# Performance work log

Hardware: AMD Instinct MI355X
Metric: run time of the kernel (lower is better)

Reference implementation:

```python
import jax, jax.numpy as jnp
import numpy as np

N_NODES = 100000
N_EDGES = 1600000
IN_C, HID_C, OUT_C = 128, 128, 64


def gcn_conv(x, src, dst, W, b, num_nodes):
    # PyG GCNConv: add self-loops, symmetric normalization, linear transform,
    # aggregate source features into targets.
    h = x @ W  # [N, C_out]
    loop = jnp.arange(num_nodes, dtype=src.dtype)
    s = jnp.concatenate([src, loop])
    d = jnp.concatenate([dst, loop])
    deg = jax.ops.segment_sum(jnp.ones_like(d, dtype=h.dtype), d, num_segments=num_nodes)
    inv_sqrt = jnp.where(deg > 0, jax.lax.rsqrt(deg), 0.0)
    norm = inv_sqrt[s] * inv_sqrt[d]  # [E+N]
    msgs = h[s] * norm[:, None]  # gather + scale
    out = jax.ops.segment_sum(msgs, d, num_segments=num_nodes)  # scatter-add
    return out + b


def setup_inputs() -> dict:
    key = jax.random.key(0)
    k1, k2, k3, k4 = jax.random.split(key, 4)
    x = jax.random.normal(k1, (N_NODES, IN_C), dtype=jnp.float32)
    edge_index = jax.random.randint(k2, (2, N_EDGES), 0, N_NODES, dtype=jnp.int64)
    W1 = jax.random.normal(k3, (IN_C, HID_C), dtype=jnp.float32) * (1.0 / np.sqrt(IN_C))
    b1 = jnp.zeros((HID_C,), dtype=jnp.float32)
    W2 = jax.random.normal(k4, (HID_C, OUT_C), dtype=jnp.float32) * (1.0 / np.sqrt(HID_C))
    b2 = jnp.zeros((OUT_C,), dtype=jnp.float32)
    return {"x": x, "edge_index": edge_index, "W1": W1, "b1": b1, "W2": W2, "b2": b2}


def reference(x, edge_index, W1, b1, W2, b2):
    num_nodes = x.shape[0]
    src, dst = edge_index[0], edge_index[1]  # PyG flow: source -> target
    h = gcn_conv(x, src, dst, W1, b1, num_nodes)
    h = jax.nn.relu(h)  # dropout is identity in eval mode
    out = gcn_conv(h, src, dst, W2, b2, num_nodes)
    return out
```

## Files before the change

kernel.cpp:

```cpp
#include <hip/hip_runtime.h>

#define IN_C 128
#define HID_C 128
#define OUT_C 64

#define BSPAN 256
#define BCAP  5120
#define NBMAX 512
#define ACHUNK 4096

typedef unsigned int uint32;
typedef unsigned short ushort16;
typedef _Float16 f16;
typedef f16   f16x8 __attribute__((ext_vector_type(8)));
typedef float f32x4 __attribute__((ext_vector_type(4)));


__device__ __forceinline__ ushort16 f2bf(float f) {
    union { float f; uint32 u; } v; v.f = f;
    uint32 r = v.u + 0x7FFFu + ((v.u >> 16) & 1u);
    return (ushort16)(r >> 16);
}

__device__ __forceinline__ void unpack2(uint32 u, float& f0, float& f1) {
    union { uint32 x; float f; } a, b;
    a.x = u << 16;
    b.x = u & 0xFFFF0000u;
    f0 = a.f; f1 = b.f;
}


__launch_bounds__(256)
__global__ void bin_edges_kernel(const int* __restrict__ src, const int* __restrict__ dst,
                                 int* __restrict__ bucketCur, uint32* __restrict__ binned,
                                 int E, int nbuck) {
    __shared__ int hist[NBMAX];
    __shared__ int base[NBMAX];
    __shared__ int rank[NBMAX];
    const int tid = threadIdx.x;
    const int e0  = blockIdx.x * ACHUNK;

    for (int i = tid; i < NBMAX; i += 256) { hist[i] = 0; rank[i] = 0; }
    __syncthreads();

    int d[16], s[16];
#pragma unroll
    for (int j = 0; j < 16; j++) {
        int e = e0 + j * 256 + tid;
        if (e < E) {
            d[j] = dst[e];
            s[j] = src[e];
            atomicAdd(&hist[d[j] >> 8], 1);
        } else d[j] = -1;
    }
    __syncthreads();

    for (int b = tid; b < nbuck; b += 256) {
        int h = hist[b];
        base[b] = h ? atomicAdd(&bucketCur[b], h) : 0;
    }
    __syncthreads();

#pragma unroll
    for (int j = 0; j < 16; j++) {
        if (d[j] >= 0) {
            int b = d[j] >> 8;
            int r = atomicAdd(&rank[b], 1);
            int pos = base[b] + r;
            if (pos < BCAP)
                binned[(size_t)b * BCAP + pos] =
                    ((uint32)(d[j] & 255) << 17) | (uint32)s[j];
        }
    }
}


__launch_bounds__(256)
__global__ void bucket_csr_kernel(const uint32* __restrict__ binned,
                                  const int* __restrict__ bucketCur,
                                  int* __restrict__ csr_src, int* __restrict__ rowbeg,
                                  int* __restrict__ rowend, float* __restrict__ inv, int N) {
    __shared__ int cnt[BSPAN];
    __shared__ int scn[BSPAN];
    __shared__ int cur[BSPAN];
    const int b   = blockIdx.x;
    const int tid = threadIdx.x;
    const int n0  = b * BSPAN;
    const int ne  = min(bucketCur[b], BCAP);
    const uint32* bp = binned + (size_t)b * BCAP;

    cnt[tid] = 0;
    __syncthreads();
    for (int i = tid; i < ne; i += 256)
        atomicAdd(&cnt[bp[i] >> 17], 1);
    __syncthreads();

    int v = cnt[tid];
    scn[tid] = v;
    __syncthreads();
    for (int off = 1; off < 256; off <<= 1) {
        int u = (tid >= off) ? scn[tid - off] : 0;
        __syncthreads();
        scn[tid] += u;
        __syncthreads();
    }
    int excl = scn[tid] - v;
    cur[tid] = excl;

    int n = n0 + tid;
    if (n < N) {
        int gb = b * BCAP + excl;
        rowbeg[n] = gb;
        rowend[n] = gb + v;
        inv[n] = rsqrtf((float)(v + 1));
    }
    __syncthreads();

    for (int i = tid; i < ne; i += 256) {
        uint32 e = bp[i];
        int r = atomicAdd(&cur[e >> 17], 1);
        csr_src[(size_t)b * BCAP + r] = (int)(e & 0x1FFFFu);
    }
}


template <int C>
__global__ void wprep_kernel(const float* __restrict__ W, f16* __restrict__ Wf) {
    constexpr int NCT = C / 16;
    int t = blockIdx.x * 256 + threadIdx.x;
    if (t >= 4 * NCT * 64) return;
    int lane = t & 63;
    int ctkc = t >> 6;
    int ct = ctkc % NCT, kc = ctkc / NCT;
    int kbase = kc * 32 + (lane >> 4) * 8;
    int col   = ct * 16 + (lane & 15);
    f16 v[8];
#pragma unroll
    for (int j = 0; j < 8; j++) v[j] = (f16)W[(size_t)(kbase + j) * C + col];
    *(uint4*)(Wf + (size_t)t * 8) = *(const uint4*)v;
}


template <int C, bool AF16>
__launch_bounds__(256)
__global__ void mfma_gemm(const void* __restrict__ Xv, const f16* __restrict__ Wf,
                          const float* __restrict__ inv, ushort16* __restrict__ outb, int N) {
    constexpr int NCT = C / 16;
    __shared__ __align__(16) f16 As[4 * 4 * 64 * 8];
    __shared__ __align__(16) f16 Bs[4 * NCT * 64 * 8];

    const int tid  = threadIdx.x;
    const int lane = tid & 63;
    const int w    = tid >> 6;
    const int row0 = blockIdx.x * 64;

    {
        constexpr int TOT = 4 * NCT * 64 * 8;
        const uint4* src = (const uint4*)Wf;
        uint4* dst = (uint4*)Bs;
#pragma unroll
        for (int i = 0; i < TOT / 8 / 256; i++)
            dst[tid + i * 256] = src[tid + i * 256];
    }

    {
        int r   = tid >> 2;
        int seg = tid & 3;
        int row = row0 + r;
        int ws_ = r >> 4;
        int r15 = r & 15;
        if (!AF16) {
            const float* X = (const float*)Xv;
#pragma unroll
            for (int i = 0; i < 8; i++) {
                int k = seg * 32 + i * 4;
                float4 v = make_float4(0.f, 0.f, 0.f, 0.f);
                if (row < N) v = *(const float4*)(X + (size_t)row * 128 + k);
                int q = (k >> 3) & 3, j0 = k & 7;
                f16 h[4] = {(f16)v.x, (f16)v.y, (f16)v.z, (f16)v.w};
                int slot = ((seg * 4 + ws_) * 64 + (q * 16 + r15)) * 8 + j0;
                *(uint2*)(As + slot) = *(const uint2*)h;
            }
        } else {
            const f16* X = (const f16*)Xv;
#pragma unroll
            for (int i = 0; i < 4; i++) {
                int k = seg * 32 + i * 8;
                uint4 v = make_uint4(0, 0, 0, 0);
                if (row < N) v = *(const uint4*)(X + (size_t)row * 128 + k);
                int q = (k >> 3) & 3;
                int slot = ((seg * 4 + ws_) * 64 + (q * 16 + r15)) * 8;
                *(uint4*)(As + slot) = v;
            }
        }
    }
    __syncthreads();

    f32x4 acc[NCT];
#pragma unroll
    for (int c = 0; c < NCT; c++) acc[c] = (f32x4){0.f, 0.f, 0.f, 0.f};

#pragma unroll
    for (int kc = 0; kc < 4; kc++) {
        f16x8 a = *(const f16x8*)&As[((kc * 4 + w) * 64 + lane) * 8];
#pragma unroll
        for (int ct = 0; ct < NCT; ct++) {
            f16x8 b = *(const f16x8*)&Bs[((kc * NCT + ct) * 64 + lane) * 8];
            acc[ct] = __builtin_amdgcn_mfma_f32_16x16x32_f16(a, b, acc[ct], 0, 0, 0);
        }
    }

    __syncthreads();
    ushort16* Ds = (ushort16*)As;
    const int q = lane >> 4;
    float iv[4];
#pragma unroll
    for (int reg = 0; reg < 4; reg++) {
        int row = row0 + w * 16 + q * 4 + reg;
        iv[reg] = (row < N) ? inv[row] : 0.f;
    }
#pragma unroll
    for (int ct = 0; ct < NCT; ct++) {
#pragma unroll
        for (int reg = 0; reg < 4; reg++) {
            int r = w * 16 + q * 4 + reg;
            Ds[r * C + ct * 16 + (lane & 15)] = f2bf(acc[ct][reg] * iv[reg]);
        }
    }
    __syncthreads();
    {
        int r  = tid >> 2;
        int row = row0 + r;
        if (row < N) {
            constexpr int SPT = C / 4;
            int c0 = (tid & 3) * SPT;
            const uint4* s = (const uint4*)&Ds[r * C + c0];
            uint4* d = (uint4*)(outb + (size_t)row * C + c0);
#pragma unroll
            for (int i = 0; i < SPT / 8; i++) d[i] = s[i];
        }
    }
}


template <int C, bool RELU, bool F16OUT>
__launch_bounds__(256)
__global__ void gather_agg_bf16(const int* __restrict__ rowbeg, const int* __restrict__ rowend,
                                const int* __restrict__ csr_src,
                                const ushort16* __restrict__ hsb, const float* __restrict__ inv,
                                const float* __restrict__ b, void* __restrict__ outv, int N) {
    constexpr int TPN = C / 8;
    constexpr int NPB = 256 / TPN;
    int n    = blockIdx.x * NPB + threadIdx.x / TPN;
    int lane = threadIdx.x % TPN;
    if (n >= N) return;
    int c8 = lane * 8;

    float acc[8];
    {
        uint4 raw = *(const uint4*)(hsb + (size_t)n * C + c8);
        unpack2(raw.x, acc[0], acc[1]);
        unpack2(raw.y, acc[2], acc[3]);
        unpack2(raw.z, acc[4], acc[5]);
        unpack2(raw.w, acc[6], acc[7]);
    }

    int beg = rowbeg[n];
    int end = rowend[n];
    int i = beg;
    for (; i + 2 <= end; i += 2) {
        int s0 = csr_src[i];
        int s1 = csr_src[i + 1];
        uint4 r0 = *(const uint4*)(hsb + (size_t)s0 * C + c8);
        uint4 r1 = *(const uint4*)(hsb + (size_t)s1 * C + c8);
        float f0, f1;
        unpack2(r0.x, f0, f1); acc[0] += f0; acc[1] += f1;
        unpack2(r0.y, f0, f1); acc[2] += f0; acc[3] += f1;
        unpack2(r0.z, f0, f1); acc[4] += f0; acc[5] += f1;
        unpack2(r0.w, f0, f1); acc[6] += f0; acc[7] += f1;
        unpack2(r1.x, f0, f1); acc[0] += f0; acc[1] += f1;
        unpack2(r1.y, f0, f1); acc[2] += f0; acc[3] += f1;
        unpack2(r1.z, f0, f1); acc[4] += f0; acc[5] += f1;
        unpack2(r1.w, f0, f1); acc[6] += f0; acc[7] += f1;
    }
    if (i < end) {
        int s0 = csr_src[i];
        uint4 r0 = *(const uint4*)(hsb + (size_t)s0 * C + c8);
        float f0, f1;
        unpack2(r0.x, f0, f1); acc[0] += f0; acc[1] += f1;
        unpack2(r0.y, f0, f1); acc[2] += f0; acc[3] += f1;
        unpack2(r0.z, f0, f1); acc[4] += f0; acc[5] += f1;
        unpack2(r0.w, f0, f1); acc[6] += f0; acc[7] += f1;
    }

    float iv = inv[n];
    float4 b0 = *(const float4*)(b + c8);
    float4 b1 = *(const float4*)(b + c8 + 4);
    float r[8];
    r[0] = fmaf(iv, acc[0], b0.x); r[1] = fmaf(iv, acc[1], b0.y);
    r[2] = fmaf(iv, acc[2], b0.z); r[3] = fmaf(iv, acc[3], b0.w);
    r[4] = fmaf(iv, acc[4], b1.x); r[5] = fmaf(iv, acc[5], b1.y);
    r[6] = fmaf(iv, acc[6], b1.z); r[7] = fmaf(iv, acc[7], b1.w);
    if (RELU) {
#pragma unroll
        for (int j = 0; j < 8; j++) r[j] = fmaxf(r[j], 0.f);
    }
    if (F16OUT) {
        f16 o[8];
#pragma unroll
        for (int j = 0; j < 8; j++) o[j] = (f16)r[j];
        *(uint4*)((f16*)outv + (size_t)n * C + c8) = *(const uint4*)o;
    } else {
        float* po = (float*)outv + (size_t)n * C + c8;
        *(float4*)(po)     = make_float4(r[0], r[1], r[2], r[3]);
        *(float4*)(po + 4) = make_float4(r[4], r[5], r[6], r[7]);
    }
}

extern "C" void kernel_launch(void* const* d_in, const int* in_sizes, int n_in,
                              void* d_out, int out_size, void* d_ws, size_t ws_size,
                              hipStream_t stream) {
    const float* x  = (const float*)d_in[0];
    const int*   ei = (const int*)d_in[1];
    const float* W1 = (const float*)d_in[2];
    const float* b1 = (const float*)d_in[3];
    const float* W2 = (const float*)d_in[4];
    const float* b2 = (const float*)d_in[5];
    float* out = (float*)d_out;

    const int N = in_sizes[0] / IN_C;
    const int E = in_sizes[1] / 2;
    const int* src = ei;
    const int* dst = ei + E;
    const int nbuck = (N + BSPAN - 1) / BSPAN;

    char* ws = (char*)d_ws;
    auto align_up = [](size_t v) { return (v + 1023) & ~(size_t)1023; };
    size_t off = 0;
    int*      bucketCur = (int*)(ws + off);      off += align_up((size_t)nbuck * sizeof(int));
    float*    inv       = (float*)(ws + off);    off += align_up((size_t)N * sizeof(float));
    int*      rowbeg    = (int*)(ws + off);      off += align_up((size_t)N * sizeof(int));
    int*      rowend    = (int*)(ws + off);      off += align_up((size_t)N * sizeof(int));
    uint32*   binned    = (uint32*)(ws + off);   off += align_up((size_t)nbuck * BCAP * sizeof(uint32));
    int*      csrs      = (int*)(ws + off);      off += align_up((size_t)nbuck * BCAP * sizeof(int));
    f16*      Wf1       = (f16*)(ws + off);      off += align_up((size_t)4 * (HID_C/16) * 64 * 8 * sizeof(f16));
    f16*      Wf2       = (f16*)(ws + off);      off += align_up((size_t)4 * (OUT_C/16) * 64 * 8 * sizeof(f16));
    ushort16* hs1b      = (ushort16*)(ws + off); off += align_up((size_t)N * HID_C * sizeof(ushort16));
    f16*      h1post    = (f16*)(ws + off);      off += align_up((size_t)N * HID_C * sizeof(f16));
    ushort16* hs2b      = (ushort16*)(ws + off); off += align_up((size_t)N * OUT_C * sizeof(ushort16));

    hipMemsetAsync(bucketCur, 0, (size_t)nbuck * sizeof(int), stream);
    wprep_kernel<HID_C><<<(4 * (HID_C/16) * 64 + 255) / 256, 256, 0, stream>>>(W1, Wf1);
    wprep_kernel<OUT_C><<<(4 * (OUT_C/16) * 64 + 255) / 256, 256, 0, stream>>>(W2, Wf2);
    bin_edges_kernel<<<(E + ACHUNK - 1) / ACHUNK, 256, 0, stream>>>(
        src, dst, bucketCur, binned, E, nbuck);
    bucket_csr_kernel<<<nbuck, 256, 0, stream>>>(
        binned, bucketCur, csrs, rowbeg, rowend, inv, N);

    mfma_gemm<HID_C, false><<<(N + 63) / 64, 256, 0, stream>>>(x, Wf1, inv, hs1b, N);
    {
        constexpr int NPB = 256 / (HID_C / 8);
        gather_agg_bf16<HID_C, true, true><<<(N + NPB - 1) / NPB, 256, 0, stream>>>(
            rowbeg, rowend, csrs, hs1b, inv, b1, h1post, N);
    }

    mfma_gemm<OUT_C, true><<<(N + 63) / 64, 256, 0, stream>>>(h1post, Wf2, inv, hs2b, N);
    {
        constexpr int NPB = 256 / (OUT_C / 8);
        gather_agg_bf16<OUT_C, false, false><<<(N + NPB - 1) / NPB, 256, 0, stream>>>(
            rowbeg, rowend, csrs, hs2b, inv, b2, out, N);
    }
}
```

Measured before the change: 271.6 us.

## Reuse atomic ranks in binning and CSR, merge weight prep, unroll gather by four

The binning kernel now keeps the rank returned by the histogram atomic, which removes the second shared-memory atomic pass. The bucket CSR kernel buffers each thread's edges and ranks in registers, so it skips re-reading the binned array and the second atomic pass. The two weight-prep launches are merged into one kernel, and the gather loop is unrolled to four rows per step to keep more loads in flight. The per-thread buffers (20 entries) add register pressure, and edge order within a row becomes nondeterministic, which can slightly change float summation order.

```diff
diff --git a/kernel.cpp b/kernel.cpp
--- a/kernel.cpp
+++ b/kernel.cpp
@@ -36,21 +36,20 @@
                                  int E, int nbuck) {
     __shared__ int hist[NBMAX];
     __shared__ int base[NBMAX];
-    __shared__ int rank[NBMAX];
     const int tid = threadIdx.x;
     const int e0  = blockIdx.x * ACHUNK;
 
-    for (int i = tid; i < NBMAX; i += 256) { hist[i] = 0; rank[i] = 0; }
-    __syncthreads();
-
-    int d[16], s[16];
+    for (int i = tid; i < NBMAX; i += 256) hist[i] = 0;
+    __syncthreads();
+
+    int d[16], s[16], rk[16];
 #pragma unroll
     for (int j = 0; j < 16; j++) {
         int e = e0 + j * 256 + tid;
         if (e < E) {
             d[j] = dst[e];
             s[j] = src[e];
-            atomicAdd(&hist[d[j] >> 8], 1);
+            rk[j] = atomicAdd(&hist[d[j] >> 8], 1);
         } else d[j] = -1;
     }
     __syncthreads();
@@ -65,8 +64,7 @@
     for (int j = 0; j < 16; j++) {
         if (d[j] >= 0) {
             int b = d[j] >> 8;
-            int r = atomicAdd(&rank[b], 1);
-            int pos = base[b] + r;
+            int pos = base[b] + rk[j];
             if (pos < BCAP)
                 binned[(size_t)b * BCAP + pos] =
                     ((uint32)(d[j] & 255) << 17) | (uint32)s[j];
@@ -80,9 +78,10 @@
                                   const int* __restrict__ bucketCur,
                                   int* __restrict__ csr_src, int* __restrict__ rowbeg,
                                   int* __restrict__ rowend, float* __restrict__ inv, int N) {
+    constexpr int MAXIT = BCAP / 256;
     __shared__ int cnt[BSPAN];
     __shared__ int scn[BSPAN];
-    __shared__ int cur[BSPAN];
+    __shared__ int excl[BSPAN];
     const int b   = blockIdx.x;
     const int tid = threadIdx.x;
     const int n0  = b * BSPAN;
@@ -91,8 +90,16 @@
 
     cnt[tid] = 0;
     __syncthreads();
-    for (int i = tid; i < ne; i += 256)
-        atomicAdd(&cnt[bp[i] >> 17], 1);
+
+    uint32 ebuf[MAXIT];
+    int    rbuf[MAXIT];
+    int nmine = 0;
+    for (int i = tid; i < ne; i += 256) {
+        uint32 e = bp[i];
+        ebuf[nmine] = e;
+        rbuf[nmine] = atomicAdd(&cnt[e >> 17], 1);
+        nmine++;
+    }
     __syncthreads();
 
     int v = cnt[tid];
@@ -104,31 +111,28 @@
         scn[tid] += u;
         __syncthreads();
     }
-    int excl = scn[tid] - v;
-    cur[tid] = excl;
+    int ex = scn[tid] - v;
+    excl[tid] = ex;
 
     int n = n0 + tid;
     if (n < N) {
-        int gb = b * BCAP + excl;
+        int gb = b * BCAP + ex;
         rowbeg[n] = gb;
         rowend[n] = gb + v;
         inv[n] = rsqrtf((float)(v + 1));
     }
     __syncthreads();
 
-    for (int i = tid; i < ne; i += 256) {
-        uint32 e = bp[i];
-        int r = atomicAdd(&cur[e >> 17], 1);
-        csr_src[(size_t)b * BCAP + r] = (int)(e & 0x1FFFFu);
+    for (int j = 0; j < nmine; j++) {
+        uint32 e = ebuf[j];
+        csr_src[(size_t)b * BCAP + excl[e >> 17] + rbuf[j]] = (int)(e & 0x1FFFFu);
     }
 }
 
 
 template <int C>
-__global__ void wprep_kernel(const float* __restrict__ W, f16* __restrict__ Wf) {
+__device__ __forceinline__ void wprep_one(const float* __restrict__ W, f16* __restrict__ Wf, int t) {
     constexpr int NCT = C / 16;
-    int t = blockIdx.x * 256 + threadIdx.x;
-    if (t >= 4 * NCT * 64) return;
     int lane = t & 63;
     int ctkc = t >> 6;
     int ct = ctkc % NCT, kc = ctkc / NCT;
@@ -138,6 +142,15 @@
 #pragma unroll
     for (int j = 0; j < 8; j++) v[j] = (f16)W[(size_t)(kbase + j) * C + col];
     *(uint4*)(Wf + (size_t)t * 8) = *(const uint4*)v;
+}
+
+__global__ void wprep_both(const float* __restrict__ W1, f16* __restrict__ Wf1,
+                           const float* __restrict__ W2, f16* __restrict__ Wf2) {
+    constexpr int T1 = 4 * (HID_C / 16) * 64;
+    constexpr int T2 = 4 * (OUT_C / 16) * 64;
+    int t = blockIdx.x * 256 + threadIdx.x;
+    if (t < T1)            wprep_one<HID_C>(W1, Wf1, t);
+    else if (t < T1 + T2)  wprep_one<OUT_C>(W2, Wf2, t - T1);
 }
 
 
@@ -242,6 +255,14 @@
     }
 }
 
+
+__device__ __forceinline__ void acc_row(uint4 r, float* acc) {
+    float f0, f1;
+    unpack2(r.x, f0, f1); acc[0] += f0; acc[1] += f1;
+    unpack2(r.y, f0, f1); acc[2] += f0; acc[3] += f1;
+    unpack2(r.z, f0, f1); acc[4] += f0; acc[5] += f1;
+    unpack2(r.w, f0, f1); acc[6] += f0; acc[7] += f1;
+}
 
 template <int C, bool RELU, bool F16OUT>
 __launch_bounds__(256)
@@ -268,29 +289,21 @@
     int beg = rowbeg[n];
     int end = rowend[n];
     int i = beg;
-    for (; i + 2 <= end; i += 2) {
+    for (; i + 4 <= end; i += 4) {
         int s0 = csr_src[i];
         int s1 = csr_src[i + 1];
+        int s2 = csr_src[i + 2];
+        int s3 = csr_src[i + 3];
         uint4 r0 = *(const uint4*)(hsb + (size_t)s0 * C + c8);
         uint4 r1 = *(const uint4*)(hsb + (size_t)s1 * C + c8);
-        float f0, f1;
-        unpack2(r0.x, f0, f1); acc[0] += f0; acc[1] += f1;
-        unpack2(r0.y, f0, f1); acc[2] += f0; acc[3] += f1;
-        unpack2(r0.z, f0, f1); acc[4] += f0; acc[5] += f1;
-        unpack2(r0.w, f0, f1); acc[6] += f0; acc[7] += f1;
-        unpack2(r1.x, f0, f1); acc[0] += f0; acc[1] += f1;
-        unpack2(r1.y, f0, f1); acc[2] += f0; acc[3] += f1;
-        unpack2(r1.z, f0, f1); acc[4] += f0; acc[5] += f1;
-        unpack2(r1.w, f0, f1); acc[6] += f0; acc[7] += f1;
-    }
-    if (i < end) {
+        uint4 r2 = *(const uint4*)(hsb + (size_t)s2 * C + c8);
+        uint4 r3 = *(const uint4*)(hsb + (size_t)s3 * C + c8);
+        acc_row(r0, acc); acc_row(r1, acc); acc_row(r2, acc); acc_row(r3, acc);
+    }
+    for (; i < end; i++) {
         int s0 = csr_src[i];
         uint4 r0 = *(const uint4*)(hsb + (size_t)s0 * C + c8);
-        float f0, f1;
-        unpack2(r0.x, f0, f1); acc[0] += f0; acc[1] += f1;
-        unpack2(r0.y, f0, f1); acc[2] += f0; acc[3] += f1;
-        unpack2(r0.z, f0, f1); acc[4] += f0; acc[5] += f1;
-        unpack2(r0.w, f0, f1); acc[6] += f0; acc[7] += f1;
+        acc_row(r0, acc);
     }
 
     float iv = inv[n];
@@ -350,8 +363,7 @@
     ushort16* hs2b      = (ushort16*)(ws + off); off += align_up((size_t)N * OUT_C * sizeof(ushort16));
 
     hipMemsetAsync(bucketCur, 0, (size_t)nbuck * sizeof(int), stream);
-    wprep_kernel<HID_C><<<(4 * (HID_C/16) * 64 + 255) / 256, 256, 0, stream>>>(W1, Wf1);
-    wprep_kernel<OUT_C><<<(4 * (OUT_C/16) * 64 + 255) / 256, 256, 0, stream>>>(W2, Wf2);
+    wprep_both<<<(4 * (HID_C/16 + OUT_C/16) * 64 + 255) / 256, 256, 0, stream>>>(W1, Wf1, W2, Wf2);
     bin_edges_kernel<<<(E + ACHUNK - 1) / ACHUNK, 256, 0, stream>>>(
         src, dst, bucketCur, binned, E, nbuck);
     bucket_csr_kernel<<<nbuck, 256, 0, stream>>>(
```

Measured after the change: 267.8 us. About the same (-1.4%).
